# Optimization experiments

Measured on AMD Instinct MI355X. Metric: run time of the kernel, lower is better.

The kernel has to match this reference:

```python
import jax, jax.numpy as jnp
import numpy as np
import math

B, CIN, H, W = 32, 128, 64, 64
COUT, KH, KW = 256, 3, 3


def setup_inputs() -> dict:
    key = jax.random.key(0)
    k1, k2, k3 = jax.random.split(key, 3)
    sqrtk = math.sqrt(1.0 / (CIN * KH * KW))
    x = jax.random.normal(k1, (B, CIN, H, W), dtype=jnp.float32)
    weight = jax.random.uniform(k2, (COUT, CIN, KH, KW), dtype=jnp.float32, minval=-sqrtk, maxval=sqrtk)
    bias = jax.random.uniform(k3, (COUT,), dtype=jnp.float32, minval=-sqrtk, maxval=sqrtk)
    return {"input": x, "weight": weight, "bias": bias}


def reference(input, weight, bias):
    # VALID (no padding), stride-1 cross-correlation conv, NCHW/OIHW layout,
    # matching the original nested-loop direct convolution + per-channel bias.
    out = jax.lax.conv_general_dilated(
        input, weight,
        window_strides=(1, 1), padding='VALID',
        dimension_numbers=('NCHW', 'OIHW', 'NCHW'))
    return out + bias[None, :, None, None]
```

## Files before the change

kernel.cpp:

```cpp
#include <hip/hip_runtime.h>

#define NB   32
#define NCI  128
#define NH   64
#define NW   64
#define NCO  256
#define NOH  62
#define NOW  62

typedef __attribute__((ext_vector_type(8))) short bf16x8;
typedef __attribute__((ext_vector_type(8))) unsigned short u16x8;
typedef __attribute__((ext_vector_type(4))) float f32x4;

typedef __attribute__((address_space(1))) const unsigned int glb_u32_t;
typedef __attribute__((address_space(3))) unsigned int lds_u32_t;

__device__ __forceinline__ unsigned short f2bf(float f) {
  unsigned int u = __float_as_uint(f);
  u = u + 0x7FFFu + ((u >> 16) & 1u);
  return (unsigned short)(u >> 16);
}

__device__ __forceinline__ void gload_lds16(const unsigned short* g, unsigned short* l) {
  __builtin_amdgcn_global_load_lds((glb_u32_t*)g, (lds_u32_t*)l, 16, 0, 0);
}

__global__ __launch_bounds__(256) void cvt_x_kernel(const float* __restrict__ x,
                                                    unsigned short* __restrict__ xt) {
  __shared__ unsigned short l[64 * 130];
  const int tid = threadIdx.x;
  const int b = blockIdx.x >> 6, h = blockIdx.x & 63;
  const int w0 = tid & 63, c0 = tid >> 6;
  const float* src = x + ((size_t)b * NCI * NH + h) * NW;
  #pragma unroll
  for (int g = 0; g < 32; ++g) {
    int ci = g * 4 + c0;
    l[w0 * 130 + ci] = f2bf(src[(size_t)ci * (NH * NW) + w0]);
  }
  __syncthreads();
  unsigned short* dst = xt + ((size_t)b * NH + h) * NW * NCI;
  #pragma unroll
  for (int it = 0; it < 4; ++it) {
    int gidx = it * 2048 + tid * 8;
    int w = gidx >> 7, ci0 = gidx & 127;
    const unsigned int* lw = (const unsigned int*)(l + w * 130 + ci0);
    union { u16x8 v; unsigned int u[4]; } t;
    t.u[0] = lw[0]; t.u[1] = lw[1]; t.u[2] = lw[2]; t.u[3] = lw[3];
    *(u16x8*)(dst + w * NCI + ci0) = t.v;
  }
}

__global__ __launch_bounds__(256) void cvt_w_kernel(const float* __restrict__ wsrc,
                                                    unsigned short* __restrict__ wt) {
  int t = blockIdx.x * 256 + threadIdx.x;
  int oc = t & 15, co = (t >> 4) & 255, k = t >> 12;
  const float* src = wsrc + ((size_t)co * NCI + oc * 8) * 9 + k;
  u16x8 v;
  #pragma unroll
  for (int j = 0; j < 8; ++j) v[j] = f2bf(src[j * 9]);
  *(u16x8*)(wt + ((size_t)k * NCO + co) * NCI + oc * 8) = v;
}

__global__ __launch_bounds__(256, 2) void conv_mfma_kernel(
    const unsigned short* __restrict__ xt, const unsigned short* __restrict__ wt,
    const float* __restrict__ bias, float* __restrict__ out) {
  __shared__ unsigned short smem[2 * 8192 + 3 * 8192];

  const int tid  = threadIdx.x;
  const int lane = tid & 63;
  const int wid  = tid >> 6;
  const int wm   = wid & 1;
  const int wn   = wid >> 1;
  const int l15  = lane & 15;
  const int lo   = lane >> 4;

  const int bid0 = blockIdx.x;
  const int bid  = (bid0 & 7) * 124 + (bid0 >> 3);
  const int b    = bid / 31;
  const int ohg  = bid % 31;
  const int oh0  = ohg * 2;

  f32x4 acc[8][4];
  #pragma unroll
  for (int mi = 0; mi < 8; ++mi)
    #pragma unroll
    for (int ni = 0; ni < 4; ++ni)
      acc[mi][ni] = (f32x4){0.f, 0.f, 0.f, 0.f};

  const char* sm = (const char*)smem;
  const int af_lane = (wm * 128 + l15) * 64 + ((lo ^ ((l15 >> 1) & 3)) * 16);
  int bf_lane[3];
  #pragma unroll
  for (int kw = 0; kw < 3; ++kw)
    bf_lane[kw] = wn * 4096 + (l15 + kw) * 64
                + ((lo ^ (((l15 + kw) >> 1) & 3)) * 16);

  const size_t xbase = (size_t)b * NH * NW * NCI;
  const unsigned short* xsrc[4];
  const unsigned short* wsrcp[4];
  #pragma unroll
  for (int i = 0; i < 4; ++i) {
    int u = (wid * 4 + i) * 64 + lane;
    int o = u & 3, w = (u >> 2) & 63, r = u >> 8;
    xsrc[i] = xt + xbase + ((size_t)(oh0 + r) * NW + w) * NCI
            + ((o ^ ((w >> 1) & 3)) * 8);
    int v = (wid * 4 + i) * 64 + lane;
    int o2 = v & 3, co = v >> 2;
    wsrcp[i] = wt + (size_t)co * NCI + ((o2 ^ ((co >> 1) & 3)) * 8);
  }
  const int ebase = wid * 4;

  auto stage_w = [&](int c, int t) {
    unsigned short* dst = smem + 16384 + (t % 3) * 8192;
    const size_t so = (size_t)t * NCO * NCI + c * 32;
    #pragma unroll
    for (int i = 0; i < 4; ++i)
      gload_lds16(wsrcp[i] + so, dst + (ebase + i) * 512);
  };
  auto stage_x = [&](int c) {
    unsigned short* dst = smem + (c & 1) * 8192;
    #pragma unroll
    for (int i = 0; i < 4; ++i)
      gload_lds16(xsrc[i] + c * 32, dst + (ebase + i) * 512);
  };

  stage_w(0, 0);
  stage_x(0);
  stage_w(0, 1);

  for (int cic = 0; cic < 4; ++cic) {
    const int xoff = (cic & 1) * 16384;
    #pragma unroll
    for (int tap = 0; tap < 9; ++tap) {
      const int kh = tap / 3, kw = tap % 3;

      if (tap == 8) {
        if (cic == 3) { asm volatile("s_waitcnt vmcnt(0)" ::: "memory"); }
        else          { asm volatile("s_waitcnt vmcnt(8)" ::: "memory"); }
      } else {
        asm volatile("s_waitcnt vmcnt(4)" ::: "memory");
      }
      __builtin_amdgcn_s_barrier();
      __builtin_amdgcn_sched_barrier(0);

      bf16x8 af[8], bfv[4];
      #pragma unroll
      for (int mi = 0; mi < 8; ++mi)
        af[mi] = *(const bf16x8*)(sm + 32768 + (tap % 3) * 16384
                                  + mi * 1024 + af_lane);
      #pragma unroll
      for (int ni = 0; ni < 4; ++ni)
        bfv[ni] = *(const bf16x8*)(sm + xoff + kh * 4096 + ni * 1024
                                   + bf_lane[kw]);

      if (tap <= 6) {
        stage_w(cic, tap + 2);
      } else if (tap == 7) {
        if (cic < 3) { stage_w(cic + 1, 0); stage_x(cic + 1); }
      } else {
        if (cic < 3) stage_w(cic + 1, 1);
      }

      __builtin_amdgcn_s_setprio(1);
      #pragma unroll
      for (int mi = 0; mi < 8; ++mi)
        #pragma unroll
        for (int ni = 0; ni < 4; ++ni)
          acc[mi][ni] = __builtin_amdgcn_mfma_f32_16x16x32_bf16(
              af[mi], bfv[ni], acc[mi][ni], 0, 0, 0);
      __builtin_amdgcn_s_setprio(0);
    }
  }

  const int oh = oh0 + wn;
  #pragma unroll
  for (int mi = 0; mi < 8; ++mi) {
    int co0 = wm * 128 + mi * 16 + lo * 4;
    const f32x4 bv = *(const f32x4*)(bias + co0);
    #pragma unroll
    for (int ni = 0; ni < 4; ++ni) {
      int ow = ni * 16 + l15;
      if (ow < NOW) {
        size_t o0 = (((size_t)b * NCO + co0) * NOH + oh) * NOW + ow;
        const size_t cs = (size_t)NOH * NOW;
        out[o0]          = acc[mi][ni][0] + bv[0];
        out[o0 + cs]     = acc[mi][ni][1] + bv[1];
        out[o0 + 2 * cs] = acc[mi][ni][2] + bv[2];
        out[o0 + 3 * cs] = acc[mi][ni][3] + bv[3];
      }
    }
  }
}

__global__ __launch_bounds__(256) void conv_naive_kernel(
    const float* __restrict__ x, const float* __restrict__ w,
    const float* __restrict__ bias, float* __restrict__ out) {
  long t = (long)blockIdx.x * 256 + threadIdx.x;
  const long total = (long)NB * NCO * NOH * NOW;
  if (t >= total) return;
  int ow = (int)(t % NOW);
  int oh = (int)((t / NOW) % NOH);
  int co = (int)((t / ((long)NOW * NOH)) % NCO);
  int b  = (int)(t / ((long)NOW * NOH * NCO));
  float acc = bias[co];
  for (int ci = 0; ci < NCI; ++ci) {
    const float* xp = x + (((size_t)b * NCI + ci) * NH + oh) * NW + ow;
    const float* wp = w + ((size_t)co * NCI + ci) * 9;
    #pragma unroll
    for (int kh = 0; kh < 3; ++kh)
      #pragma unroll
      for (int kw = 0; kw < 3; ++kw)
        acc += xp[kh * NW + kw] * wp[kh * 3 + kw];
  }
  out[t] = acc;
}

extern "C" void kernel_launch(void* const* d_in, const int* in_sizes, int n_in,
                              void* d_out, int out_size, void* d_ws, size_t ws_size,
                              hipStream_t stream) {
  const float* x    = (const float*)d_in[0];
  const float* w    = (const float*)d_in[1];
  const float* bias = (const float*)d_in[2];
  float* out        = (float*)d_out;

  const size_t WT_BYTES = (size_t)9 * NCO * NCI * 2;
  const size_t XT_BYTES = (size_t)NB * NH * NW * NCI * 2;

  if (ws_size >= WT_BYTES + XT_BYTES) {
    unsigned short* wt = (unsigned short*)d_ws;
    unsigned short* xt = (unsigned short*)((char*)d_ws + WT_BYTES);
    cvt_w_kernel<<<(9 * NCO * 16) / 256, 256, 0, stream>>>(w, wt);
    cvt_x_kernel<<<NB * NH, 256, 0, stream>>>(x, xt);
    conv_mfma_kernel<<<31 * NB, 256, 0, stream>>>(xt, wt, bias, out);
  } else {
    const long total = (long)NB * NCO * NOH * NOW;
    conv_naive_kernel<<<(int)((total + 255) / 256), 256, 0, stream>>>(x, w, bias, out);
  }
}
```

Baseline: 97.95 us.

## Retile conv MFMA kernel to 128-channel by 4-row blocks with 4-deep weight pipeline

Each block now covers 128 output channels and 4 output rows instead of all 256 channels and 2 rows. Each wave handles one output row, and the block stages 6 input rows per 32-channel chunk. Weights stream through a 4-slot ring, and taps are processed in pairs with one barrier and a full vmcnt(0) wait per pair. The grid grows from 992 to 1024 blocks, and the last row group clamps its loads and skips the out-of-range row (rows 62-63 of the 64 computed). The goal is better input-row reuse and finer-grained work, at the cost of reloading each input tile for both channel halves and a coarser wait pattern.

```diff
diff --git a/kernel.cpp b/kernel.cpp
--- a/kernel.cpp
+++ b/kernel.cpp
@@ -64,21 +64,22 @@
 __global__ __launch_bounds__(256, 2) void conv_mfma_kernel(
     const unsigned short* __restrict__ xt, const unsigned short* __restrict__ wt,
     const float* __restrict__ bias, float* __restrict__ out) {
-  __shared__ unsigned short smem[2 * 8192 + 3 * 8192];
+  __shared__ unsigned short smem[40960];
 
   const int tid  = threadIdx.x;
   const int lane = tid & 63;
   const int wid  = tid >> 6;
-  const int wm   = wid & 1;
-  const int wn   = wid >> 1;
+  const int wn   = wid;
   const int l15  = lane & 15;
   const int lo   = lane >> 4;
 
-  const int bid0 = blockIdx.x;
-  const int bid  = (bid0 & 7) * 124 + (bid0 >> 3);
-  const int b    = bid / 31;
-  const int ohg  = bid % 31;
-  const int oh0  = ohg * 2;
+  const int bid0  = blockIdx.x;
+  const int bid   = (bid0 & 7) * 128 + (bid0 >> 3);
+  const int coutg = bid & 1;
+  const int ohg   = (bid >> 1) & 15;
+  const int b     = bid >> 5;
+  const int cbase = coutg * 128;
+  const int oh0   = ohg * 4;
 
   f32x4 acc[8][4];
   #pragma unroll
@@ -88,105 +89,110 @@
       acc[mi][ni] = (f32x4){0.f, 0.f, 0.f, 0.f};
 
   const char* sm = (const char*)smem;
-  const int af_lane = (wm * 128 + l15) * 64 + ((lo ^ ((l15 >> 1) & 3)) * 16);
-  int bf_lane[3];
-  #pragma unroll
-  for (int kw = 0; kw < 3; ++kw)
-    bf_lane[kw] = wn * 4096 + (l15 + kw) * 64
-                + ((lo ^ (((l15 + kw) >> 1) & 3)) * 16);
+  const int af_lane = l15 * 64 + ((lo ^ ((l15 >> 1) & 3)) << 4);
 
   const size_t xbase = (size_t)b * NH * NW * NCI;
-  const unsigned short* xsrc[4];
-  const unsigned short* wsrcp[4];
-  #pragma unroll
-  for (int i = 0; i < 4; ++i) {
-    int u = (wid * 4 + i) * 64 + lane;
-    int o = u & 3, w = (u >> 2) & 63, r = u >> 8;
-    xsrc[i] = xt + xbase + ((size_t)(oh0 + r) * NW + w) * NCI
+  const unsigned short* xsrc[6];
+  #pragma unroll
+  for (int i = 0; i < 6; ++i) {
+    int e = (wid * 6 + i) * 64 + lane;
+    int o = e & 3, w = (e >> 2) & 63, r = e >> 8;
+    int row = oh0 + r; if (row > 63) row = 63;
+    xsrc[i] = xt + xbase + ((size_t)row * NW + w) * NCI
             + ((o ^ ((w >> 1) & 3)) * 8);
-    int v = (wid * 4 + i) * 64 + lane;
-    int o2 = v & 3, co = v >> 2;
-    wsrcp[i] = wt + (size_t)co * NCI + ((o2 ^ ((co >> 1) & 3)) * 8);
-  }
-  const int ebase = wid * 4;
-
-  auto stage_w = [&](int c, int t) {
-    unsigned short* dst = smem + 16384 + (t % 3) * 8192;
-    const size_t so = (size_t)t * NCO * NCI + c * 32;
-    #pragma unroll
-    for (int i = 0; i < 4; ++i)
-      gload_lds16(wsrcp[i] + so, dst + (ebase + i) * 512);
+  }
+  const unsigned short* wsrc2[2];
+  #pragma unroll
+  for (int i = 0; i < 2; ++i) {
+    int e = (wid * 2 + i) * 64 + lane;
+    int o = e & 3, co = e >> 2;
+    wsrc2[i] = wt + (size_t)(cbase + co) * NCI + ((o ^ ((co >> 1) & 3)) * 8);
+  }
+
+  auto stage_w = [&](int bufq, int t9, int c) {
+    unsigned short* dst = smem + 24576 + bufq * 4096;
+    const size_t so = (size_t)t9 * NCO * NCI + c * 32;
+    #pragma unroll
+    for (int i = 0; i < 2; ++i)
+      gload_lds16(wsrc2[i] + so, dst + ((wid * 2 + i) * 64 + lane) * 8);
   };
   auto stage_x = [&](int c) {
-    unsigned short* dst = smem + (c & 1) * 8192;
-    #pragma unroll
-    for (int i = 0; i < 4; ++i)
-      gload_lds16(xsrc[i] + c * 32, dst + (ebase + i) * 512);
+    unsigned short* dst = smem + (c & 1) * 12288;
+    #pragma unroll
+    for (int i = 0; i < 6; ++i)
+      gload_lds16(xsrc[i] + c * 32, dst + ((wid * 6 + i) * 64 + lane) * 8);
   };
 
-  stage_w(0, 0);
+  auto tap_compute = [&](int bufq, int t9, int c) {
+    const int kh = t9 / 3, kw = t9 % 3;
+    const int r  = wn + kh;
+    const int w9 = l15 + kw;
+    const int bfl = w9 * 64 + ((lo ^ ((w9 >> 1) & 3)) << 4);
+    const char* wsp = sm + 49152 + bufq * 8192;
+    const char* xsp = sm + (c & 1) * 24576 + r * 4096;
+    bf16x8 af[8], bfv[4];
+    #pragma unroll
+    for (int mi = 0; mi < 8; ++mi)
+      af[mi] = *(const bf16x8*)(wsp + mi * 1024 + af_lane);
+    #pragma unroll
+    for (int ni = 0; ni < 4; ++ni)
+      bfv[ni] = *(const bf16x8*)(xsp + ni * 1024 + bfl);
+    __builtin_amdgcn_s_setprio(1);
+    #pragma unroll
+    for (int mi = 0; mi < 8; ++mi)
+      #pragma unroll
+      for (int ni = 0; ni < 4; ++ni)
+        acc[mi][ni] = __builtin_amdgcn_mfma_f32_16x16x32_bf16(
+            af[mi], bfv[ni], acc[mi][ni], 0, 0, 0);
+    __builtin_amdgcn_s_setprio(0);
+  };
+
+  stage_w(0, 0, 0);
+  stage_w(1, 1, 0);
   stage_x(0);
-  stage_w(0, 1);
-
-  for (int cic = 0; cic < 4; ++cic) {
-    const int xoff = (cic & 1) * 16384;
-    #pragma unroll
-    for (int tap = 0; tap < 9; ++tap) {
-      const int kh = tap / 3, kw = tap % 3;
-
-      if (tap == 8) {
-        if (cic == 3) { asm volatile("s_waitcnt vmcnt(0)" ::: "memory"); }
-        else          { asm volatile("s_waitcnt vmcnt(8)" ::: "memory"); }
-      } else {
-        asm volatile("s_waitcnt vmcnt(4)" ::: "memory");
-      }
+
+  for (int h = 0; h < 9; ++h) {
+    #pragma unroll
+    for (int jp = 0; jp < 2; ++jp) {
+      const int ta  = h * 4 + jp * 2;
+      const int tb  = ta + 1;
+      const int t9a = ta % 9, ca = ta / 9;
+      const int t9b = tb % 9, cb = tb / 9;
+      const int qa  = jp * 2, qb = jp * 2 + 1;
+      const int qa2 = (jp * 2 + 2) & 3, qb2 = (jp * 2 + 3) & 3;
+
+      asm volatile("s_waitcnt vmcnt(0)" ::: "memory");
       __builtin_amdgcn_s_barrier();
       __builtin_amdgcn_sched_barrier(0);
 
-      bf16x8 af[8], bfv[4];
+      tap_compute(qa, t9a, ca);
+
+      if (ta + 2 <= 35) stage_w(qa2, (ta + 2) % 9, (ta + 2) / 9);
+      if (tb + 2 <= 35) stage_w(qb2, (tb + 2) % 9, (tb + 2) / 9);
+      if (t9a == 4 && ca < 3) stage_x(ca + 1);
+      if (t9b == 4 && cb < 3) stage_x(cb + 1);
+
+      tap_compute(qb, t9b, cb);
+    }
+  }
+
+  const int oh = oh0 + wn;
+  if (oh < NOH) {
+    #pragma unroll
+    for (int mi = 0; mi < 8; ++mi) {
+      int co0 = cbase + mi * 16 + lo * 4;
+      const f32x4 bv = *(const f32x4*)(bias + co0);
       #pragma unroll
-      for (int mi = 0; mi < 8; ++mi)
-        af[mi] = *(const bf16x8*)(sm + 32768 + (tap % 3) * 16384
-                                  + mi * 1024 + af_lane);
-      #pragma unroll
-      for (int ni = 0; ni < 4; ++ni)
-        bfv[ni] = *(const bf16x8*)(sm + xoff + kh * 4096 + ni * 1024
-                                   + bf_lane[kw]);
-
-      if (tap <= 6) {
-        stage_w(cic, tap + 2);
-      } else if (tap == 7) {
-        if (cic < 3) { stage_w(cic + 1, 0); stage_x(cic + 1); }
-      } else {
-        if (cic < 3) stage_w(cic + 1, 1);
-      }
-
-      __builtin_amdgcn_s_setprio(1);
-      #pragma unroll
-      for (int mi = 0; mi < 8; ++mi)
-        #pragma unroll
-        for (int ni = 0; ni < 4; ++ni)
-          acc[mi][ni] = __builtin_amdgcn_mfma_f32_16x16x32_bf16(
-              af[mi], bfv[ni], acc[mi][ni], 0, 0, 0);
-      __builtin_amdgcn_s_setprio(0);
-    }
-  }
-
-  const int oh = oh0 + wn;
-  #pragma unroll
-  for (int mi = 0; mi < 8; ++mi) {
-    int co0 = wm * 128 + mi * 16 + lo * 4;
-    const f32x4 bv = *(const f32x4*)(bias + co0);
-    #pragma unroll
-    for (int ni = 0; ni < 4; ++ni) {
-      int ow = ni * 16 + l15;
-      if (ow < NOW) {
-        size_t o0 = (((size_t)b * NCO + co0) * NOH + oh) * NOW + ow;
-        const size_t cs = (size_t)NOH * NOW;
-        out[o0]          = acc[mi][ni][0] + bv[0];
-        out[o0 + cs]     = acc[mi][ni][1] + bv[1];
-        out[o0 + 2 * cs] = acc[mi][ni][2] + bv[2];
-        out[o0 + 3 * cs] = acc[mi][ni][3] + bv[3];
+      for (int ni = 0; ni < 4; ++ni) {
+        int ow = ni * 16 + l15;
+        if (ow < NOW) {
+          size_t o0 = (((size_t)b * NCO + co0) * NOH + oh) * NOW + ow;
+          const size_t cs = (size_t)NOH * NOW;
+          out[o0]          = acc[mi][ni][0] + bv[0];
+          out[o0 + cs]     = acc[mi][ni][1] + bv[1];
+          out[o0 + 2 * cs] = acc[mi][ni][2] + bv[2];
+          out[o0 + 3 * cs] = acc[mi][ni][3] + bv[3];
+        }
       }
     }
   }
@@ -231,7 +237,7 @@
     unsigned short* xt = (unsigned short*)((char*)d_ws + WT_BYTES);
     cvt_w_kernel<<<(9 * NCO * 16) / 256, 256, 0, stream>>>(w, wt);
     cvt_x_kernel<<<NB * NH, 256, 0, stream>>>(x, xt);
-    conv_mfma_kernel<<<31 * NB, 256, 0, stream>>>(xt, wt, bias, out);
+    conv_mfma_kernel<<<2 * 16 * NB, 256, 0, stream>>>(xt, wt, bias, out);
   } else {
     const long total = (long)NB * NCO * NOH * NOW;
     conv_naive_kernel<<<(int)((total + 255) / 256), 256, 0, stream>>>(x, w, bias, out);
```

Result: slower. 101.0 us (+3.1%).
